# Kernel tuning notes

Hardware: AMD Instinct MI355X
Metric: run time of the kernel (lower is better)

The kernel has to match this reference:

```python
import jax, jax.numpy as jnp
import numpy as np

EPS = 0.1
SHAPE = (1, 1, 96, 96)  # [B, C, H, W]


def setup_inputs() -> dict:
    key = jax.random.key(0)
    x = jax.random.normal(key, SHAPE, dtype=jnp.float32)
    return {"x": x}


def reference(x):
    eps = EPS
    B, C, H, W = x.shape
    N = C * H * W  # max possible new error terms; buffer grows to 1 + N slots

    # clip the eps-ball into [0, 1]: bias shifts, error radius shrinks
    r_low = jax.nn.relu(eps - x) * 0.5
    r_high = jax.nn.relu(x - (1.0 - eps)) * 0.5
    bias = x + r_low - r_high                  # zonotope center, [B,C,H,W]
    err = eps - r_low - r_high                 # per-pixel error magnitude

    ef = err.reshape(N)
    cond = ef >= 0                             # which pixels get an error term
    # stream compaction: k-th true condition -> error-term slot 1+k (slot 0 = bias)
    slot = jnp.cumsum(cond.astype(jnp.int32))  # 1-based compacted index
    err_idx = jnp.where(cond, slot, N + 1)     # out-of-range -> dropped

    f, i, j = jnp.unravel_index(jnp.arange(N), (C, H, W))

    zono = jnp.zeros((B, 1 + N, C, H, W), dtype=x.dtype)
    zono = zono.at[0, 0].set(bias[0])
    zono = zono.at[0, err_idx, f, i, j].set(ef, mode='drop')
    return zono
```

## Files before the change

### kernel.cpp

```cpp
#include <hip/hip_runtime.h>

#define NPIX 9216
#define NROWS (NPIX + 1)
#define ROW4 (NPIX / 4)
#define EPSV 0.1f

#define FILL_BLOCKS 2592
#define ITERS 32

typedef float f32x4 __attribute__((ext_vector_type(4)));

__global__ __launch_bounds__(256) void fill_kernel(const float* __restrict__ x,
                                                   f32x4* __restrict__ out) {
    const int b   = blockIdx.x;
    const int tid = threadIdx.x;

    if (b < FILL_BLOCKS) {
        const f32x4 z = {0.0f, 0.0f, 0.0f, 0.0f};
        f32x4* p = out + ROW4 + (long long)b * (256 * ITERS) + tid;
#pragma unroll
        for (int it = 0; it < ITERS; ++it) {
            p[0] = z;
            p += 256;
        }
    } else {
        const f32x4* x4 = reinterpret_cast<const f32x4*>(x);
#pragma unroll
        for (int it = 0; it < 9; ++it) {
            const int c4 = tid + it * 256;
            const f32x4 xv = x4[c4];
            f32x4 o;
#pragma unroll
            for (int d = 0; d < 4; ++d) {
                const float v = xv[d];
                o[d] = v + fmaxf(EPSV - v, 0.0f) * 0.5f
                         - fmaxf(v - (1.0f - EPSV), 0.0f) * 0.5f;
            }
            out[c4] = o;
        }
    }
}

__global__ __launch_bounds__(1024) void finish_kernel(const float* __restrict__ x,
                                                      float* __restrict__ out) {
    __shared__ int wsum[16];
    const int tid  = threadIdx.x;
    const int lane = tid & 63;
    const int wid  = tid >> 6;
    const int base = tid * 9;

    float e_loc[9];
    int   c_loc[9];
    int   cnt = 0;
#pragma unroll
    for (int k = 0; k < 9; ++k) {
        const float xv     = x[base + k];
        const float r_low  = fmaxf(EPSV - xv, 0.0f) * 0.5f;
        const float r_high = fmaxf(xv - (1.0f - EPSV), 0.0f) * 0.5f;
        const float e      = EPSV - r_low - r_high;
        e_loc[k] = e;
        c_loc[k] = (e >= 0.0f) ? 1 : 0;
        cnt += c_loc[k];
    }

    int v = cnt;
#pragma unroll
    for (int off = 1; off < 64; off <<= 1) {
        const int t = __shfl_up(v, off, 64);
        if (lane >= off) v += t;
    }
    if (lane == 63) wsum[wid] = v;
    __syncthreads();

    int woff = 0;
#pragma unroll
    for (int w = 0; w < 16; ++w) woff += (w < wid) ? wsum[w] : 0;

    int slot = woff + v - cnt;
#pragma unroll
    for (int k = 0; k < 9; ++k) {
        if (c_loc[k]) {
            ++slot;
            out[(long long)slot * NPIX + (base + k)] = e_loc[k];
        }
    }
}

extern "C" void kernel_launch(void* const* d_in, const int* in_sizes, int n_in,
                              void* d_out, int out_size, void* d_ws, size_t ws_size,
                              hipStream_t stream) {
    const float* x = (const float*)d_in[0];
    float* out = (float*)d_out;

    fill_kernel<<<FILL_BLOCKS + 1, 256, 0, stream>>>(x, (f32x4*)out);
    finish_kernel<<<1, 1024, 0, stream>>>(x, out);
}
```

Before: 67.87 us.

## Fuse diagonal scatter into zero-fill blocks with per-block redundant prefix scan

Merges the separate single-block finish kernel into the fill kernel. Every fill block recomputes the whole error vector and its prefix-sum compaction over all 9216 pixels. It then writes only the diagonal entries whose flat index falls inside the chunk it just zeroed, ordered after the zero stores by the block's barrier. This removes the second launch and the serial tail of a lone 1024-thread block, at the cost of each of the 2592 blocks redundantly reading all of x and doing the scan.

```diff
diff --git a/kernel.cpp b/kernel.cpp
--- a/kernel.cpp
+++ b/kernel.cpp
@@ -7,24 +7,19 @@
 
 #define FILL_BLOCKS 2592
 #define ITERS 32
+#define CHUNK4 (256 * ITERS)
+#define CHUNKF (CHUNK4 * 4)
 
 typedef float f32x4 __attribute__((ext_vector_type(4)));
 
-__global__ __launch_bounds__(256) void fill_kernel(const float* __restrict__ x,
-                                                   f32x4* __restrict__ out) {
+__global__ __launch_bounds__(256) void zono_kernel(const float* __restrict__ x,
+                                                   float* __restrict__ out) {
     const int b   = blockIdx.x;
     const int tid = threadIdx.x;
+    f32x4* out4 = reinterpret_cast<f32x4*>(out);
+    const f32x4* x4 = reinterpret_cast<const f32x4*>(x);
 
-    if (b < FILL_BLOCKS) {
-        const f32x4 z = {0.0f, 0.0f, 0.0f, 0.0f};
-        f32x4* p = out + ROW4 + (long long)b * (256 * ITERS) + tid;
-#pragma unroll
-        for (int it = 0; it < ITERS; ++it) {
-            p[0] = z;
-            p += 256;
-        }
-    } else {
-        const f32x4* x4 = reinterpret_cast<const f32x4*>(x);
+    if (b == FILL_BLOCKS) {
 #pragma unroll
         for (int it = 0; it < 9; ++it) {
             const int c4 = tid + it * 256;
@@ -36,32 +31,41 @@
                 o[d] = v + fmaxf(EPSV - v, 0.0f) * 0.5f
                          - fmaxf(v - (1.0f - EPSV), 0.0f) * 0.5f;
             }
-            out[c4] = o;
+            out4[c4] = o;
+        }
+        return;
+    }
+
+    {
+        const f32x4 z = {0.0f, 0.0f, 0.0f, 0.0f};
+        f32x4* p = out4 + ROW4 + b * CHUNK4 + tid;
+#pragma unroll
+        for (int it = 0; it < ITERS; ++it) {
+            p[0] = z;
+            p += 256;
         }
     }
-}
 
-__global__ __launch_bounds__(1024) void finish_kernel(const float* __restrict__ x,
-                                                      float* __restrict__ out) {
-    __shared__ int wsum[16];
-    const int tid  = threadIdx.x;
+    f32x4 e_loc[9];
+    int cnt = 0;
+#pragma unroll
+    for (int i = 0; i < 9; ++i) {
+        const f32x4 xv = x4[tid * 9 + i];
+        f32x4 ev;
+#pragma unroll
+        for (int d = 0; d < 4; ++d) {
+            const float v  = xv[d];
+            const float rl = fmaxf(EPSV - v, 0.0f) * 0.5f;
+            const float rh = fmaxf(v - (1.0f - EPSV), 0.0f) * 0.5f;
+            ev[d] = EPSV - rl - rh;
+            cnt += (ev[d] >= 0.0f) ? 1 : 0;
+        }
+        e_loc[i] = ev;
+    }
+
     const int lane = tid & 63;
     const int wid  = tid >> 6;
-    const int base = tid * 9;
-
-    float e_loc[9];
-    int   c_loc[9];
-    int   cnt = 0;
-#pragma unroll
-    for (int k = 0; k < 9; ++k) {
-        const float xv     = x[base + k];
-        const float r_low  = fmaxf(EPSV - xv, 0.0f) * 0.5f;
-        const float r_high = fmaxf(xv - (1.0f - EPSV), 0.0f) * 0.5f;
-        const float e      = EPSV - r_low - r_high;
-        e_loc[k] = e;
-        c_loc[k] = (e >= 0.0f) ? 1 : 0;
-        cnt += c_loc[k];
-    }
+    __shared__ int wsum[4];
 
     int v = cnt;
 #pragma unroll
@@ -74,14 +78,22 @@
 
     int woff = 0;
 #pragma unroll
-    for (int w = 0; w < 16; ++w) woff += (w < wid) ? wsum[w] : 0;
+    for (int w = 0; w < 4; ++w) woff += (w < wid) ? wsum[w] : 0;
 
     int slot = woff + v - cnt;
+    const int floatLo = NPIX + b * CHUNKF;
+    const int floatHi = floatLo + CHUNKF;
+    const int pbase = tid * 36;
 #pragma unroll
-    for (int k = 0; k < 9; ++k) {
-        if (c_loc[k]) {
-            ++slot;
-            out[(long long)slot * NPIX + (base + k)] = e_loc[k];
+    for (int i = 0; i < 9; ++i) {
+#pragma unroll
+        for (int d = 0; d < 4; ++d) {
+            const float e = e_loc[i][d];
+            if (e >= 0.0f) {
+                ++slot;
+                const int c = slot * NPIX + (pbase + i * 4 + d);
+                if (c >= floatLo && c < floatHi) out[c] = e;
+            }
         }
     }
 }
@@ -92,6 +104,5 @@
     const float* x = (const float*)d_in[0];
     float* out = (float*)d_out;
 
-    fill_kernel<<<FILL_BLOCKS + 1, 256, 0, stream>>>(x, (f32x4*)out);
-    finish_kernel<<<1, 1024, 0, stream>>>(x, out);
+    zono_kernel<<<FILL_BLOCKS + 1, 256, 0, stream>>>(x, out);
 }
```

After: 68.29 us. About the same (+0.6%).
